# Kernel optimization log

Hardware: AMD Instinct MI355X
Metric: run time of the kernel (lower is better)

The kernel has to match this reference:

```python
import jax, jax.numpy as jnp
import numpy as np

D = 1024       # hidden_dim
H = 16         # n_heads
HD = D // H    # head dim = 64
V = 32000      # vocab_size
S = 4          # n_scales
IT = 6         # iters_per_scale
L = S * IT     # total_layers = 24 (one shared block, looped)
G = 16         # n_rot_groups
g = D // G     # group dim = 64
FF = 4 * D     # ff_mult * hidden_dim
N_TRI = g * (g - 1) // 2  # 2016 upper-tri skew params per group
EPS = 1e-6


def rmsnorm(x, w):
    return x * jax.lax.rsqrt(jnp.mean(x * x, axis=-1, keepdims=True) + EPS) * w


def setup_inputs() -> dict:
    key = jax.random.key(0)
    ks = jax.random.split(key, 12)
    rn = lambda k, shape, s: jax.random.normal(k, shape, jnp.float32) * s
    return {
        "tokens": jax.random.randint(ks[0], (1, 1024), 0, V),
        "embed_w": rn(ks[1], (V, D), 0.02),
        "lm_head_w": rn(ks[2], (V, D), 0.02),
        "norm_w": jnp.ones((D,), jnp.float32),
        "layer_gamma": 1.0 + rn(ks[3], (L, D), 0.02),
        "layer_beta": rn(ks[4], (L, D), 0.02),
        "iter_scale": 1.0 + rn(ks[5], (S, IT), 0.02),
        "skew_upper": rn(ks[6], (L, G, N_TRI), 0.02),
        "ln1_w": jnp.ones((D,), jnp.float32),
        "ln2_w": jnp.ones((D,), jnp.float32),
        "wqkv": rn(ks[7], (D, 3 * D), 0.02),
        "wo": rn(ks[8], (D, D), 0.02),
        "w1": rn(ks[9], (D, FF), 0.02),
        "w2": rn(ks[10], (FF, D), 0.02),
    }


def _rotations(skew_upper):
    """Cayley transform per layer/group: R = (I - A/2)^-1 (I + A/2), A skew-symm."""
    rows, cols = np.triu_indices(g, k=1)
    def one_layer(su):  # su: (G, N_TRI)
        A = jnp.zeros((G, g, g), su.dtype).at[:, rows, cols].set(su)
        A = A - jnp.swapaxes(A, -1, -2)
        I = jnp.eye(g, dtype=su.dtype)
        return jnp.linalg.solve(I - 0.5 * A, I + 0.5 * A)  # (G, g, g)
    return jax.vmap(one_layer)(skew_upper)  # (L, G, g, g)


def _block(x, gamma, beta, ln1_w, ln2_w, wqkv, wo, w1, w2):
    """Pre-norm causal transformer block with (gamma, beta) affine modulation."""
    B, T, _ = x.shape
    h = rmsnorm(x, ln1_w) * gamma + beta
    qkv = h @ wqkv  # (B, T, 3D)
    q, k, v = jnp.split(qkv, 3, axis=-1)
    q = q.reshape(B, T, H, HD)
    k = k.reshape(B, T, H, HD)
    v = v.reshape(B, T, H, HD)
    scores = jnp.einsum('bqhd,bkhd->bhqk', q, k) / np.sqrt(HD).astype(np.float32)
    causal = jnp.tril(jnp.ones((T, T), bool))
    scores = jnp.where(causal, scores, jnp.float32(-1e9))
    attn = jax.nn.softmax(scores, axis=-1)
    attn_out = jnp.einsum('bhqk,bkhd->bqhd', attn, v).reshape(B, T, D) @ wo
    x = x + attn_out
    x = x + jax.nn.gelu(rmsnorm(x, ln2_w) @ w1) @ w2
    return x


def reference(tokens, embed_w, lm_head_w, norm_w, layer_gamma, layer_beta,
              iter_scale, skew_upper, ln1_w, ln2_w, wqkv, wo, w1, w2):
    B, T = tokens.shape
    x = embed_w[tokens].astype(jnp.float32)  # (B, T, D)
    R = _rotations(skew_upper)               # (L, G, g, g)
    its = iter_scale.reshape(-1)             # (L,) scale index order matches loop
    for l in range(L):
        blk = _block(x, layer_gamma[l], layer_beta[l], ln1_w, ln2_w, wqkv, wo, w1, w2)
        x = x + (blk - x) * its[l]           # affine residual blend
        xg = x.reshape(B, T, G, g)
        x = jnp.einsum('btgi,gij->btgj', xg, R[l]).reshape(B, T, D)  # group rotation
    x = rmsnorm(x, norm_w)
    return x @ lm_head_w.T                   # (B, T, V) logits
```

## Files before the change

### kernel.cpp

```cpp
#include <hip/hip_runtime.h>
#include <hip/hip_bf16.h>
#include <math.h>

constexpr int kD = 1024;
constexpr int kH = 16;
constexpr int kV = 32000;
constexpr int kT = 1024;
constexpr int kG = 16;
constexpr int kFF = 4096;
constexpr int kL = 24;
constexpr int kNTRI = 2016;
#define EPSF 1e-6f
#define L2E 1.44269504088896f

typedef __bf16 bf16x8 __attribute__((ext_vector_type(8)));
typedef __bf16 bf16x4 __attribute__((ext_vector_type(4)));
typedef float f32x4 __attribute__((ext_vector_type(4)));

#define GLOAD16(g, l)                                                   \
  __builtin_amdgcn_global_load_lds(                                     \
      (const __attribute__((address_space(1))) void*)(g),               \
      (__attribute__((address_space(3))) void*)(l), 16, 0, 0)

__global__ __launch_bounds__(256) void cayley_kernel(const float* __restrict__ skew,
                                                     float* __restrict__ R) {
  int lg = blockIdx.x;
  int tid = threadIdx.x;
  int r = tid & 63, q = tid >> 6;
  __shared__ float Ms[64][65];
  __shared__ float Bs[64][65];
  const float* su = skew + (size_t)lg * kNTRI;
#pragma unroll
  for (int cc = 0; cc < 16; ++cc) {
    int c = q * 16 + cc;
    float a = 0.f;
    if (r < c) a = su[r * (127 - r) / 2 + (c - r - 1)];
    else if (r > c) a = -su[c * (127 - c) / 2 + (r - c - 1)];
    Ms[r][c] = (r == c ? 1.f : 0.f) - 0.5f * a;
    Bs[r][c] = (r == c ? 1.f : 0.f) + 0.5f * a;
  }
  __syncthreads();
  for (int k = 0; k < 64; ++k) {
    float ip = 1.f / Ms[k][k];
    float f = Ms[r][k];
    float beta = (r == k) ? (1.f - ip) : (f * ip);
    float mk[16], bk[16];
#pragma unroll
    for (int cc = 0; cc < 16; ++cc) {
      mk[cc] = Ms[k][q * 16 + cc];
      bk[cc] = Bs[k][q * 16 + cc];
    }
    __syncthreads();
#pragma unroll
    for (int cc = 0; cc < 16; ++cc) {
      int c = q * 16 + cc;
      Ms[r][c] -= beta * mk[cc];
      Bs[r][c] -= beta * bk[cc];
    }
    __syncthreads();
  }
  float* Ro = R + ((size_t)lg * 64 + r) * 64;
#pragma unroll
  for (int cc = 0; cc < 16; ++cc) Ro[q * 16 + cc] = Bs[r][q * 16 + cc];
}

__global__ __launch_bounds__(256) void embed_kernel(const int* __restrict__ tok,
                                                    const float* __restrict__ ew,
                                                    float* __restrict__ x) {
  int i = blockIdx.x * 256 + threadIdx.x;
  int t = i >> 8;
  int d4 = i & 255;
  int v = tok[t];
  reinterpret_cast<float4*>(x)[i] =
      reinterpret_cast<const float4*>(ew + (size_t)v * kD)[d4];
}

__global__ __launch_bounds__(256) void cast_kernel(const float* __restrict__ W,
                                                   __bf16* __restrict__ O) {
  size_t i = ((size_t)blockIdx.x * 256 + threadIdx.x) * 8;
  float4 f0 = *reinterpret_cast<const float4*>(W + i);
  float4 f1 = *reinterpret_cast<const float4*>(W + i + 4);
  bf16x8 v;
  v[0] = (__bf16)f0.x; v[1] = (__bf16)f0.y;
  v[2] = (__bf16)f0.z; v[3] = (__bf16)f0.w;
  v[4] = (__bf16)f1.x; v[5] = (__bf16)f1.y;
  v[6] = (__bf16)f1.z; v[7] = (__bf16)f1.w;
  *reinterpret_cast<bf16x8*>(O + i) = v;
}

__global__ __launch_bounds__(256) void convt_kernel(const float* __restrict__ W,
                                                    __bf16* __restrict__ WT,
                                                    int K, int N) {
  __shared__ float tile[64][65];
  int t = threadIdx.x;
  int n0 = blockIdx.x * 64, k0 = blockIdx.y * 64;
#pragma unroll
  for (int r = 0; r < 4; ++r) {
    int kr = r * 16 + (t >> 4);
    int nc = (t & 15) * 4;
    float4 v = *reinterpret_cast<const float4*>(&W[(size_t)(k0 + kr) * N + n0 + nc]);
    tile[kr][nc + 0] = v.x;
    tile[kr][nc + 1] = v.y;
    tile[kr][nc + 2] = v.z;
    tile[kr][nc + 3] = v.w;
  }
  __syncthreads();
#pragma unroll
  for (int r = 0; r < 2; ++r) {
    int idx = r * 256 + t;
    int nrow = idx >> 3, kc = (idx & 7) * 8;
    bf16x8 v;
#pragma unroll
    for (int j = 0; j < 8; ++j) v[j] = (__bf16)tile[kc + j][nrow];
    *reinterpret_cast<bf16x8*>(&WT[(size_t)(n0 + nrow) * K + k0 + kc]) = v;
  }
}

template <bool AFFINE>
__global__ __launch_bounds__(256) void rms_kernel(const float* __restrict__ x,
                                                  const float* __restrict__ w,
                                                  const float* __restrict__ gamma,
                                                  const float* __restrict__ beta,
                                                  __bf16* __restrict__ out) {
  int t = blockIdx.x, tid = threadIdx.x;
  __shared__ float red4[4];
  float4 xv = reinterpret_cast<const float4*>(x + (size_t)t * kD)[tid];
  float ss = xv.x * xv.x + xv.y * xv.y + xv.z * xv.z + xv.w * xv.w;
#pragma unroll
  for (int o = 1; o < 64; o <<= 1) ss += __shfl_xor(ss, o);
  if ((tid & 63) == 0) red4[tid >> 6] = ss;
  __syncthreads();
  float tot = red4[0] + red4[1] + red4[2] + red4[3];
  float rms = rsqrtf(tot / (float)kD + EPSF);
  float4 wv = reinterpret_cast<const float4*>(w)[tid];
  float o0 = xv.x * rms * wv.x;
  float o1 = xv.y * rms * wv.y;
  float o2 = xv.z * rms * wv.z;
  float o3 = xv.w * rms * wv.w;
  if (AFFINE) {
    float4 gv = reinterpret_cast<const float4*>(gamma)[tid];
    float4 bv = reinterpret_cast<const float4*>(beta)[tid];
    o0 = o0 * gv.x + bv.x;
    o1 = o1 * gv.y + bv.y;
    o2 = o2 * gv.z + bv.z;
    o3 = o3 * gv.w + bv.w;
  }
  bf16x4 ov;
  ov[0] = (__bf16)o0; ov[1] = (__bf16)o1; ov[2] = (__bf16)o2; ov[3] = (__bf16)o3;
  *reinterpret_cast<bf16x4*>(out + (size_t)t * kD + tid * 4) = ov;
}

__global__ __launch_bounds__(256) void rms_red_kernel(const float* __restrict__ x,
                                                      const float* __restrict__ p0,
                                                      const float* __restrict__ p1,
                                                      const float* __restrict__ w,
                                                      float* __restrict__ y,
                                                      __bf16* __restrict__ hb) {
  int t = blockIdx.x, tid = threadIdx.x;
  __shared__ float red4[4];
  size_t base = (size_t)t * kD;
  float4 xv = reinterpret_cast<const float4*>(x + base)[tid];
  float4 a = reinterpret_cast<const float4*>(p0 + base)[tid];
  float4 b = reinterpret_cast<const float4*>(p1 + base)[tid];
  float4 yv;
  yv.x = xv.x + a.x + b.x;
  yv.y = xv.y + a.y + b.y;
  yv.z = xv.z + a.z + b.z;
  yv.w = xv.w + a.w + b.w;
  reinterpret_cast<float4*>(y + base)[tid] = yv;
  float ss = yv.x * yv.x + yv.y * yv.y + yv.z * yv.z + yv.w * yv.w;
#pragma unroll
  for (int o = 1; o < 64; o <<= 1) ss += __shfl_xor(ss, o);
  if ((tid & 63) == 0) red4[tid >> 6] = ss;
  __syncthreads();
  float tot = red4[0] + red4[1] + red4[2] + red4[3];
  float rms = rsqrtf(tot / (float)kD + EPSF);
  float4 wv = reinterpret_cast<const float4*>(w)[tid];
  bf16x4 ov;
  ov[0] = (__bf16)(yv.x * rms * wv.x);
  ov[1] = (__bf16)(yv.y * rms * wv.y);
  ov[2] = (__bf16)(yv.z * rms * wv.z);
  ov[3] = (__bf16)(yv.w * rms * wv.w);
  *reinterpret_cast<bf16x4*>(hb + base + tid * 4) = ov;
}

template <int BM, int BN, int NW, int EPI, bool BF32, int KSPLIT = 1, bool DBUF = false>
__global__ __launch_bounds__(NW * 64) void gemm_kernel(
    const __bf16* __restrict__ A, const void* __restrict__ Bv,
    const float* res, void* __restrict__ Cv, int M, int N, int K) {
  constexpr int WCOLS = (NW == 4) ? 2 : 4;
  constexpr int FM = (BM / 2) / 16;
  constexpr int FN = (BN / WCOLS) / 16;
  constexpr int AISS = BM / 8 / NW;
  constexpr int BISS = BN / 8 / NW;
  constexpr int NI = AISS + BISS;
  __shared__ __bf16 As[(DBUF ? 2 : 1) * BM * 64];
  __shared__ __bf16 Bs[(DBUF ? 2 : 1) * BN * 64];
  char* AsB = (char*)As;
  char* BsB = (char*)Bs;
  int tid = threadIdx.x;
  int w = tid >> 6, lane = tid & 63;
  int mt = M / BM, nt = N / BN;
  int cpx = gridDim.x >> 3;
  int id = (blockIdx.x & 7) * cpx + (blockIdx.x >> 3);
  int ks_id = id / (mt * nt);
  int rem = id % (mt * nt);
  int bm = (rem % mt) * BM, bn = (rem / mt) * BN;
  int kbeg = ks_id * (K / KSPLIT), kend = kbeg + K / KSPLIT;
  int lrow = lane & 15, g = lane >> 4;
  int grow = lane >> 3;
  int gswz = ((lane & 7) ^ grow) * 8;
  int rsw = (lrow & 7) << 4;
  int wm = (NW == 4) ? (w >> 1) : (w >> 2);
  int wn = (NW == 4) ? (w & 1) : (w & 3);
  int wr = wm * (BM / 2), wc = wn * (BN / WCOLS);
  f32x4 acc[FM][FN] = {};
  const __bf16* B16 = (const __bf16*)Bv;
  const float* B32 = (const float*)Bv;

  auto stage = [&](int buf, int k0) {
#pragma unroll
    for (int i = 0; i < AISS; ++i) {
      int rbase = (i * NW + w) * 8;
      GLOAD16(&A[(size_t)(bm + rbase + grow) * K + k0 + gswz],
              &As[buf * BM * 64 + rbase * 64]);
    }
#pragma unroll
    for (int i = 0; i < BISS; ++i) {
      int rbase = (i * NW + w) * 8;
      GLOAD16(&B16[(size_t)(bn + rbase + grow) * K + k0 + gswz],
              &Bs[buf * BN * 64 + rbase * 64]);
    }
  };

  auto compute = [&](int buf) {
    int offA = buf * BM * 128, offB = buf * BN * 128;
#pragma unroll
    for (int ks = 0; ks < 2; ++ks) {
      bf16x8 af[FM], bg[FN];
#pragma unroll
      for (int i = 0; i < FM; ++i)
        af[i] = *reinterpret_cast<const bf16x8*>(
            AsB + offA + (wr + i * 16 + lrow) * 128 + ((ks * 64 + g * 16) ^ rsw));
#pragma unroll
      for (int j = 0; j < FN; ++j)
        bg[j] = *reinterpret_cast<const bf16x8*>(
            BsB + offB + (wc + j * 16 + lrow) * 128 + ((ks * 64 + g * 16) ^ rsw));
#pragma unroll
      for (int i = 0; i < FM; ++i)
#pragma unroll
        for (int j = 0; j < FN; ++j)
          acc[i][j] = __builtin_amdgcn_mfma_f32_16x16x32_bf16(af[i], bg[j],
                                                              acc[i][j], 0, 0, 0);
    }
  };

  if constexpr (DBUF && !BF32) {
    stage(0, kbeg);
    int cur = 0;
    for (int k0 = kbeg; k0 < kend; k0 += 64) {
      bool more = (k0 + 64 < kend);
      if (more) stage(cur ^ 1, k0 + 64);
      if (more) {
        if constexpr (NI == 2) asm volatile("s_waitcnt vmcnt(2)" ::: "memory");
        else if constexpr (NI == 3) asm volatile("s_waitcnt vmcnt(3)" ::: "memory");
        else if constexpr (NI == 4) asm volatile("s_waitcnt vmcnt(4)" ::: "memory");
        else if constexpr (NI == 6) asm volatile("s_waitcnt vmcnt(6)" ::: "memory");
        else asm volatile("s_waitcnt vmcnt(0)" ::: "memory");
      } else {
        asm volatile("s_waitcnt vmcnt(0)" ::: "memory");
      }
      __builtin_amdgcn_sched_barrier(0);
      __builtin_amdgcn_s_barrier();
      compute(cur);
      __builtin_amdgcn_s_barrier();
      cur ^= 1;
    }
  } else {
    for (int k0 = kbeg; k0 < kend; k0 += 64) {
      if (!BF32) {
        stage(0, k0);
      } else {
#pragma unroll
        for (int rrep = 0; rrep < BN * 8 / (NW * 64); ++rrep) {
          int cid = rrep * NW * 64 + tid;
          int row = cid >> 3, kc = (cid & 7) * 8;
          const float* src = &B32[(size_t)(bn + row) * K + k0 + kc];
          float4 f0 = *reinterpret_cast<const float4*>(src);
          float4 f1 = *reinterpret_cast<const float4*>(src + 4);
          bf16x8 v;
          v[0] = (__bf16)f0.x; v[1] = (__bf16)f0.y;
          v[2] = (__bf16)f0.z; v[3] = (__bf16)f0.w;
          v[4] = (__bf16)f1.x; v[5] = (__bf16)f1.y;
          v[6] = (__bf16)f1.z; v[7] = (__bf16)f1.w;
          int swc = ((cid & 7) ^ (row & 7)) * 16;
          *reinterpret_cast<bf16x8*>(BsB + row * 128 + swc) = v;
        }
#pragma unroll
        for (int i = 0; i < AISS; ++i) {
          int rbase = (i * NW + w) * 8;
          GLOAD16(&A[(size_t)(bm + rbase + grow) * K + k0 + gswz], &As[rbase * 64]);
        }
      }
      __syncthreads();
      compute(0);
      __syncthreads();
    }
  }

  float* Cp = (float*)Cv + (size_t)ks_id * M * N;
  int crow0 = bm + wr + g * 4;
  int ccol0 = bn + wc + lrow;
#pragma unroll
  for (int i = 0; i < FM; ++i) {
#pragma unroll
    for (int j = 0; j < FN; ++j) {
#pragma unroll
      for (int r = 0; r < 4; ++r) {
        int row = crow0 + i * 16 + r;
        int col = ccol0 + j * 16;
        size_t idx = (size_t)row * N + col;
        float v = acc[i][j][r];
        if (EPI == 1) v += res[idx];
        if (EPI == 2) {
          float u = v;
          float z = 0.7978845608028654f * (u + 0.044715f * u * u * u);
          float ez = exp2f(z * (2.f * L2E));
          v = u * ez / (1.f + ez);
        }
        if (EPI == 2 || EPI == 3) ((__bf16*)Cv)[idx] = (__bf16)v;
        else Cp[idx] = v;
      }
    }
  }
}

__global__ __launch_bounds__(256) void fattn_kernel(const __bf16* __restrict__ qkv,
                                                    __bf16* __restrict__ out) {
  __shared__ __bf16 Ks[2][64 * 64];
  __shared__ __bf16 Vt[2][64 * 64];
  __shared__ __bf16 Ps[4 * 16 * 64];
  int tid = threadIdx.x;
  int bq = blockIdx.x * 64;
  int h = blockIdx.y;
  int w = tid >> 6, lane = tid & 63;
  int g = lane >> 4, lr = lane & 15;

  bf16x8 qf[2];
  const __bf16* qbase = qkv + (size_t)(bq + w * 16 + lr) * (3 * kD) + h * 64;
#pragma unroll
  for (int ks = 0; ks < 2; ++ks) {
    bf16x8 v = *reinterpret_cast<const bf16x8*>(qbase + ks * 32 + g * 8);
#pragma unroll
    for (int j = 0; j < 8; ++j) qf[ks][j] = (__bf16)((float)v[j] * 0.125f);
  }

  f32x4 acc[4] = {};
  float m = -1e30f, lsum = 0.f;

  int srow = tid >> 2, sseg = tid & 3;
  int vk = tid & 63, vd0 = (tid >> 6) * 16;
  char* PwB = (char*)(Ps + w * (16 * 64));
  int psw = (lr & 7) << 4;

  bf16x8 ka, kb2, va, vb;
  int ntiles = bq / 64 + 1;

  {
    const __bf16* src = qkv + (size_t)(srow) * (3 * kD) + kD + h * 64 + sseg * 16;
    ka = *reinterpret_cast<const bf16x8*>(src);
    kb2 = *reinterpret_cast<const bf16x8*>(src + 8);
    const __bf16* vsrc = qkv + (size_t)(vk) * (3 * kD) + 2 * kD + h * 64 + vd0;
    va = *reinterpret_cast<const bf16x8*>(vsrc);
    vb = *reinterpret_cast<const bf16x8*>(vsrc + 8);
    char* KsB = (char*)Ks[0];
    char* VtB = (char*)Vt[0];
    int bc = sseg * 32, sw = (srow & 7) << 4;
    *reinterpret_cast<bf16x8*>(KsB + srow * 128 + (bc ^ sw)) = ka;
    *reinterpret_cast<bf16x8*>(KsB + srow * 128 + ((bc + 16) ^ sw)) = kb2;
#pragma unroll
    for (int i = 0; i < 8; ++i) {
      int d = vd0 + i;
      *((__bf16*)(VtB + d * 128 + ((vk * 2) ^ ((d & 7) << 4)))) = va[i];
      d = vd0 + 8 + i;
      *((__bf16*)(VtB + d * 128 + ((vk * 2) ^ ((d & 7) << 4)))) = vb[i];
    }
  }

  int cur = 0;
  for (int kt = 0; kt < ntiles; ++kt) {
    if (kt + 1 < ntiles) {
      const __bf16* src =
          qkv + (size_t)((kt + 1) * 64 + srow) * (3 * kD) + kD + h * 64 + sseg * 16;
      ka = *reinterpret_cast<const bf16x8*>(src);
      kb2 = *reinterpret_cast<const bf16x8*>(src + 8);
      const __bf16* vsrc =
          qkv + (size_t)((kt + 1) * 64 + vk) * (3 * kD) + 2 * kD + h * 64 + vd0;
      va = *reinterpret_cast<const bf16x8*>(vsrc);
      vb = *reinterpret_cast<const bf16x8*>(vsrc + 8);
    }
    __syncthreads();

    char* KsB = (char*)Ks[cur];
    char* VtB = (char*)Vt[cur];
    bool diag = (kt == ntiles - 1);
    int jmax = diag ? w : 3;

    f32x4 s[4];
#pragma unroll
    for (int jj = 0; jj < 4; ++jj) {
      if (jj <= jmax) {
        int krow = jj * 16 + lr;
        int ksw = (lr & 7) << 4;
        bf16x8 k0 = *reinterpret_cast<const bf16x8*>(KsB + krow * 128 + ((g * 16) ^ ksw));
        bf16x8 k1 = *reinterpret_cast<const bf16x8*>(KsB + krow * 128 + ((64 + g * 16) ^ ksw));
        f32x4 z = {};
        z = __builtin_amdgcn_mfma_f32_16x16x32_bf16(k0, qf[0], z, 0, 0, 0);
        s[jj] = __builtin_amdgcn_mfma_f32_16x16x32_bf16(k1, qf[1], z, 0, 0, 0);
      } else {
        s[jj] = f32x4{-1e30f, -1e30f, -1e30f, -1e30f};
      }
    }
    if (diag) {
#pragma unroll
      for (int r = 0; r < 4; ++r)
        if (g * 4 + r > lr) s[w][r] = -1e30f;
    }

    float mt = -1e30f;
#pragma unroll
    for (int jj = 0; jj < 4; ++jj)
#pragma unroll
      for (int r = 0; r < 4; ++r) mt = fmaxf(mt, s[jj][r]);
    mt = fmaxf(mt, __shfl_xor(mt, 16));
    mt = fmaxf(mt, __shfl_xor(mt, 32));
    float mn = fmaxf(m, mt);
    float sc = exp2f((m - mn) * L2E);
    float p[4][4];
    float rs = 0.f;
#pragma unroll
    for (int jj = 0; jj < 4; ++jj)
#pragma unroll
      for (int r = 0; r < 4; ++r) {
        float e = exp2f((s[jj][r] - mn) * L2E);
        p[jj][r] = e;
        rs += e;
      }
    rs += __shfl_xor(rs, 16);
    rs += __shfl_xor(rs, 32);
    lsum = lsum * sc + rs;
    m = mn;
#pragma unroll
    for (int r = 0; r < 4; ++r) {
      float s4 = __shfl(sc, 20 * g + r);
#pragma unroll
      for (int dt = 0; dt < 4; ++dt) acc[dt][r] *= s4;
    }

#pragma unroll
    for (int jj = 0; jj < 4; ++jj) {
      bf16x4 pv;
#pragma unroll
      for (int r = 0; r < 4; ++r) pv[r] = (__bf16)p[jj][r];
      *reinterpret_cast<bf16x4*>(PwB + lr * 128 + ((jj * 32 + g * 8) ^ psw)) = pv;
    }

    {
      bf16x8 pa0 = *reinterpret_cast<const bf16x8*>(PwB + lr * 128 + ((g * 16) ^ psw));
      bf16x8 pa1 = *reinterpret_cast<const bf16x8*>(PwB + lr * 128 + ((64 + g * 16) ^ psw));
#pragma unroll
      for (int dt = 0; dt < 4; ++dt) {
        int vrow = dt * 16 + lr;
        int vsw = (lr & 7) << 4;
        bf16x8 vb0 = *reinterpret_cast<const bf16x8*>(VtB + vrow * 128 + ((g * 16) ^ vsw));
        bf16x8 vb1 = *reinterpret_cast<const bf16x8*>(VtB + vrow * 128 + ((64 + g * 16) ^ vsw));
        acc[dt] = __builtin_amdgcn_mfma_f32_16x16x32_bf16(pa0, vb0, acc[dt], 0, 0, 0);
        acc[dt] = __builtin_amdgcn_mfma_f32_16x16x32_bf16(pa1, vb1, acc[dt], 0, 0, 0);
      }
    }
    __syncthreads();

    if (kt + 1 < ntiles) {
      char* KsN = (char*)Ks[cur ^ 1];
      char* VtN = (char*)Vt[cur ^ 1];
      int bc = sseg * 32, sw = (srow & 7) << 4;
      *reinterpret_cast<bf16x8*>(KsN + srow * 128 + (bc ^ sw)) = ka;
      *reinterpret_cast<bf16x8*>(KsN + srow * 128 + ((bc + 16) ^ sw)) = kb2;
#pragma unroll
      for (int i = 0; i < 8; ++i) {
        int d = vd0 + i;
        *((__bf16*)(VtN + d * 128 + ((vk * 2) ^ ((d & 7) << 4)))) = va[i];
        d = vd0 + 8 + i;
        *((__bf16*)(VtN + d * 128 + ((vk * 2) ^ ((d & 7) << 4)))) = vb[i];
      }
      cur ^= 1;
    }
  }

  float linv = 1.f / lsum;
#pragma unroll
  for (int r = 0; r < 4; ++r) {
    float ir = __shfl(linv, 20 * g + r);
    int row = bq + w * 16 + g * 4 + r;
#pragma unroll
    for (int dt = 0; dt < 4; ++dt)
      out[(size_t)row * kD + h * 64 + dt * 16 + lr] = (__bf16)(acc[dt][r] * ir);
  }
}

__global__ __launch_bounds__(256) void blend_rot_kernel(const float* x,
                                                        const float* y,
                                                        const float* q0,
                                                        const float* q1,
                                                        const float* iscale,
                                                        int l,
                                                        const float* __restrict__ Rall,
                                                        float* xout) {
  int tc = blockIdx.x, gr = blockIdx.y;
  int tid = threadIdx.x;
  __shared__ float Rs[64 * 64];
  __shared__ float xb[64][65];
  float s = iscale[l];
  const float* Rg = Rall + ((size_t)l * kG + gr) * 4096;
  {
    int off = tid * 16;
#pragma unroll
    for (int q2 = 0; q2 < 4; ++q2) {
      float4 rv = *reinterpret_cast<const float4*>(Rg + off + q2 * 4);
      *reinterpret_cast<float4*>(&Rs[off + q2 * 4]) = rv;
    }
  }
  int tok = tid & 63, seg = (tid >> 6) * 16;
  {
    size_t base = (size_t)(tc * 64 + tok) * kD + gr * 64 + seg;
#pragma unroll
    for (int q2 = 0; q2 < 4; ++q2) {
      float4 xv = *reinterpret_cast<const float4*>(x + base + q2 * 4);
      float4 yv = *reinterpret_cast<const float4*>(y + base + q2 * 4);
      float4 a = *reinterpret_cast<const float4*>(q0 + base + q2 * 4);
      float4 b = *reinterpret_cast<const float4*>(q1 + base + q2 * 4);
      float y0 = yv.x + a.x + b.x;
      float y1 = yv.y + a.y + b.y;
      float y2 = yv.z + a.z + b.z;
      float y3 = yv.w + a.w + b.w;
      xb[tok][seg + q2 * 4 + 0] = xv.x + (y0 - xv.x) * s;
      xb[tok][seg + q2 * 4 + 1] = xv.y + (y1 - xv.y) * s;
      xb[tok][seg + q2 * 4 + 2] = xv.z + (y2 - xv.z) * s;
      xb[tok][seg + q2 * 4 + 3] = xv.w + (y3 - xv.w) * s;
    }
  }
  __syncthreads();
  float o[16] = {};
  for (int i = 0; i < 64; ++i) {
    float xv = xb[tok][i];
#pragma unroll
    for (int d = 0; d < 16; ++d) o[d] += xv * Rs[i * 64 + seg + d];
  }
  float* outr = xout + (size_t)(tc * 64 + tok) * kD + gr * 64 + seg;
#pragma unroll
  for (int q2 = 0; q2 < 4; ++q2) {
    float4 ov = {o[q2 * 4 + 0], o[q2 * 4 + 1], o[q2 * 4 + 2], o[q2 * 4 + 3]};
    *reinterpret_cast<float4*>(outr + q2 * 4) = ov;
  }
}

extern "C" void kernel_launch(void* const* d_in, const int* in_sizes, int n_in,
                              void* d_out, int out_size, void* d_ws, size_t ws_size,
                              hipStream_t stream) {
  const int* tokens = (const int*)d_in[0];
  const float* embed_w = (const float*)d_in[1];
  const float* lm_head_w = (const float*)d_in[2];
  const float* norm_w = (const float*)d_in[3];
  const float* layer_gamma = (const float*)d_in[4];
  const float* layer_beta = (const float*)d_in[5];
  const float* iter_scale = (const float*)d_in[6];
  const float* skew_upper = (const float*)d_in[7];
  const float* ln1_w = (const float*)d_in[8];
  const float* ln2_w = (const float*)d_in[9];
  const float* wqkv = (const float*)d_in[10];
  const float* wo = (const float*)d_in[11];
  const float* w1 = (const float*)d_in[12];
  const float* w2 = (const float*)d_in[13];
  float* out = (float*)d_out;

  float* x = (float*)d_ws;
  float* y = x + (size_t)kT * kD;
  __bf16* hb = (__bf16*)(y + (size_t)kT * kD);
  __bf16* ab = hb + (size_t)kT * kD;
  float* R = (float*)(ab + (size_t)kT * kD);
  __bf16* lmhb = (__bf16*)(R + (size_t)kL * kG * 4096);
  bool ws_big = ws_size >= (size_t)(4670464 + 16384000) * 4;

  __bf16* qkvb = (__bf16*)out;
  __bf16* ffb = (__bf16*)(out + 1572864);
  __bf16* wqkvT = (__bf16*)(out + 3670016);
  __bf16* woT = (__bf16*)(out + 5242880);
  __bf16* w1T = (__bf16*)(out + 5767168);
  __bf16* w2T = (__bf16*)(out + 7864320);
  float* wop = out + 9961472;
  float* w2p = out + 12058624;

  cayley_kernel<<<kL * kG, 256, 0, stream>>>(skew_upper, R);
  embed_kernel<<<kT * kD / 4 / 256, 256, 0, stream>>>(tokens, embed_w, x);
  convt_kernel<<<dim3(3 * kD / 64, kD / 64), 256, 0, stream>>>(wqkv, wqkvT, kD, 3 * kD);
  convt_kernel<<<dim3(kD / 64, kD / 64), 256, 0, stream>>>(wo, woT, kD, kD);
  convt_kernel<<<dim3(kFF / 64, kD / 64), 256, 0, stream>>>(w1, w1T, kD, kFF);
  convt_kernel<<<dim3(kD / 64, kFF / 64), 256, 0, stream>>>(w2, w2T, kFF, kD);
  if (ws_big)
    cast_kernel<<<kV * kD / 8 / 256, 256, 0, stream>>>(lm_head_w, lmhb);

  for (int l = 0; l < kL; ++l) {
    rms_kernel<true><<<kT, 256, 0, stream>>>(x, ln1_w, layer_gamma + (size_t)l * kD,
                                             layer_beta + (size_t)l * kD, hb);
    gemm_kernel<64, 128, 8, 3, false, 1, true>
        <<<(kT / 64) * (3 * kD / 128), 512, 0, stream>>>(
        hb, wqkvT, nullptr, qkvb, kT, 3 * kD, kD);
    fattn_kernel<<<dim3(kT / 64, kH), 256, 0, stream>>>(qkvb, ab);
    gemm_kernel<64, 64, 8, 0, false, 2, true>
        <<<2 * (kT / 64) * (kD / 64), 512, 0, stream>>>(
        ab, woT, nullptr, wop, kT, kD, kD);
    rms_red_kernel<<<kT, 256, 0, stream>>>(x, wop, wop + (size_t)kT * kD, ln2_w, y, hb);
    gemm_kernel<64, 128, 8, 2, false, 1, true>
        <<<(kT / 64) * (kFF / 128), 512, 0, stream>>>(
        hb, w1T, nullptr, ffb, kT, kFF, kD);
    gemm_kernel<64, 64, 8, 0, false, 2, true>
        <<<2 * (kT / 64) * (kD / 64), 512, 0, stream>>>(
        ffb, w2T, nullptr, w2p, kT, kD, kFF);
    blend_rot_kernel<<<dim3(kT / 64, kG), 256, 0, stream>>>(
        x, y, w2p, w2p + (size_t)kT * kD, iter_scale, l, R, x);
  }

  rms_kernel<false><<<kT, 256, 0, stream>>>(x, norm_w, nullptr, nullptr, hb);
  if (ws_big)
    gemm_kernel<256, 128, 8, 0, false><<<(kT / 256) * (kV / 128), 512, 0, stream>>>(
        hb, lmhb, nullptr, out, kT, kV, kD);
  else
    gemm_kernel<128, 128, 4, 0, true><<<(kT / 128) * (kV / 128), 256, 0, stream>>>(
        hb, lm_head_w, nullptr, out, kT, kV, kD);
}
```

Before: 2.578 ms.

## Split causal attention KV range in two halves with a combine kernel

The flash attention kernel now splits each query tile's causal key range into two halves across separate blocks, writing unnormalized fp32 partial accumulators plus row max and sum to scratch. A new combine kernel merges the two halves with log-sum-exp rescaling and writes the bf16 output. Block indices are remapped so that heads are grouped per XCD, and the grid doubles to 512 blocks to balance the triangular workload. The cost is an extra kernel launch and fp32 partial traffic through global memory on every layer.

```diff
diff --git a/kernel.cpp b/kernel.cpp
--- a/kernel.cpp
+++ b/kernel.cpp
@@ -336,15 +336,36 @@
 }
 
 __global__ __launch_bounds__(256) void fattn_kernel(const __bf16* __restrict__ qkv,
-                                                    __bf16* __restrict__ out) {
+                                                    float* __restrict__ pacc,
+                                                    float* __restrict__ pm,
+                                                    float* __restrict__ pl) {
   __shared__ __bf16 Ks[2][64 * 64];
   __shared__ __bf16 Vt[2][64 * 64];
   __shared__ __bf16 Ps[4 * 16 * 64];
+  int b = blockIdx.x;
+  int xcd = b & 7, idx = b >> 3;
+  int h = xcd * 2 + (idx >> 5);
+  int rem2 = idx & 31;
+  int qt = rem2 >> 1, half = rem2 & 1;
+  int bq = qt * 64;
+  int ntk = qt + 1;
+  int kb = half ? (ntk >> 1) : 0;
+  int ke = half ? ntk : (ntk >> 1);
+  int tix = (qt * 16 + h) * 2 + half;
   int tid = threadIdx.x;
-  int bq = blockIdx.x * 64;
-  int h = blockIdx.y;
   int w = tid >> 6, lane = tid & 63;
   int g = lane >> 4, lr = lane & 15;
+
+  if (kb >= ke) {
+    float* pa = pacc + (size_t)tix * 4096;
+#pragma unroll
+    for (int i = 0; i < 16; ++i) pa[tid * 16 + i] = 0.f;
+    if (tid < 64) {
+      pm[tix * 64 + tid] = -1e30f;
+      pl[tix * 64 + tid] = 0.f;
+    }
+    return;
+  }
 
   bf16x8 qf[2];
   const __bf16* qbase = qkv + (size_t)(bq + w * 16 + lr) * (3 * kD) + h * 64;
@@ -364,13 +385,12 @@
   int psw = (lr & 7) << 4;
 
   bf16x8 ka, kb2, va, vb;
-  int ntiles = bq / 64 + 1;
 
   {
-    const __bf16* src = qkv + (size_t)(srow) * (3 * kD) + kD + h * 64 + sseg * 16;
+    const __bf16* src = qkv + (size_t)(kb * 64 + srow) * (3 * kD) + kD + h * 64 + sseg * 16;
     ka = *reinterpret_cast<const bf16x8*>(src);
     kb2 = *reinterpret_cast<const bf16x8*>(src + 8);
-    const __bf16* vsrc = qkv + (size_t)(vk) * (3 * kD) + 2 * kD + h * 64 + vd0;
+    const __bf16* vsrc = qkv + (size_t)(kb * 64 + vk) * (3 * kD) + 2 * kD + h * 64 + vd0;
     va = *reinterpret_cast<const bf16x8*>(vsrc);
     vb = *reinterpret_cast<const bf16x8*>(vsrc + 8);
     char* KsB = (char*)Ks[0];
@@ -388,8 +408,8 @@
   }
 
   int cur = 0;
-  for (int kt = 0; kt < ntiles; ++kt) {
-    if (kt + 1 < ntiles) {
+  for (int kt = kb; kt < ke; ++kt) {
+    if (kt + 1 < ke) {
       const __bf16* src =
           qkv + (size_t)((kt + 1) * 64 + srow) * (3 * kD) + kD + h * 64 + sseg * 16;
       ka = *reinterpret_cast<const bf16x8*>(src);
@@ -403,7 +423,7 @@
 
     char* KsB = (char*)Ks[cur];
     char* VtB = (char*)Vt[cur];
-    bool diag = (kt == ntiles - 1);
+    bool diag = (kt == qt);
     int jmax = diag ? w : 3;
 
     f32x4 s[4];
@@ -480,7 +500,7 @@
     }
     __syncthreads();
 
-    if (kt + 1 < ntiles) {
+    if (kt + 1 < ke) {
       char* KsN = (char*)Ks[cur ^ 1];
       char* VtN = (char*)Vt[cur ^ 1];
       int bc = sseg * 32, sw = (srow & 7) << 4;
@@ -497,14 +517,45 @@
     }
   }
 
-  float linv = 1.f / lsum;
+  float* pa = pacc + (size_t)tix * 4096;
 #pragma unroll
   for (int r = 0; r < 4; ++r) {
-    float ir = __shfl(linv, 20 * g + r);
-    int row = bq + w * 16 + g * 4 + r;
+    int row = w * 16 + g * 4 + r;
 #pragma unroll
     for (int dt = 0; dt < 4; ++dt)
-      out[(size_t)row * kD + h * 64 + dt * 16 + lr] = (__bf16)(acc[dt][r] * ir);
+      pa[row * 64 + dt * 16 + lr] = acc[dt][r];
+  }
+  if (g == 0) {
+    pm[tix * 64 + w * 16 + lr] = m;
+    pl[tix * 64 + w * 16 + lr] = lsum;
+  }
+}
+
+__global__ __launch_bounds__(256) void fattn_combine_kernel(
+    const float* __restrict__ pacc, const float* __restrict__ pm,
+    const float* __restrict__ pl, __bf16* __restrict__ ab) {
+  int qt = blockIdx.x, h = blockIdx.y;
+  int tid = threadIdx.x;
+  int row = tid >> 2, c0 = (tid & 3) * 16;
+  int t0 = (qt * 16 + h) * 2, t1 = t0 + 1;
+  float m0 = pm[t0 * 64 + row], m1 = pm[t1 * 64 + row];
+  float l0 = pl[t0 * 64 + row], l1 = pl[t1 * 64 + row];
+  float mm = fmaxf(m0, m1);
+  float e0 = exp2f((m0 - mm) * L2E), e1 = exp2f((m1 - mm) * L2E);
+  float inv = 1.f / (e0 * l0 + e1 * l1);
+  const float* a0 = pacc + (size_t)t0 * 4096 + row * 64 + c0;
+  const float* a1 = pacc + (size_t)t1 * 4096 + row * 64 + c0;
+  __bf16* o = ab + (size_t)(qt * 64 + row) * kD + h * 64 + c0;
+#pragma unroll
+  for (int c = 0; c < 16; c += 4) {
+    float4 v0 = *reinterpret_cast<const float4*>(a0 + c);
+    float4 v1 = *reinterpret_cast<const float4*>(a1 + c);
+    bf16x4 ov;
+    ov[0] = (__bf16)((e0 * v0.x + e1 * v1.x) * inv);
+    ov[1] = (__bf16)((e0 * v0.y + e1 * v1.y) * inv);
+    ov[2] = (__bf16)((e0 * v0.z + e1 * v1.z) * inv);
+    ov[3] = (__bf16)((e0 * v0.w + e1 * v1.w) * inv);
+    *reinterpret_cast<bf16x4*>(o + c) = ov;
   }
 }
 
@@ -599,6 +650,9 @@
   __bf16* w2T = (__bf16*)(out + 7864320);
   float* wop = out + 9961472;
   float* w2p = out + 12058624;
+  float* pacc = out + 14155776;
+  float* pm = out + 16252928;
+  float* pl = out + 16285696;
 
   cayley_kernel<<<kL * kG, 256, 0, stream>>>(skew_upper, R);
   embed_kernel<<<kT * kD / 4 / 256, 256, 0, stream>>>(tokens, embed_w, x);
@@ -615,7 +669,8 @@
     gemm_kernel<64, 128, 8, 3, false, 1, true>
         <<<(kT / 64) * (3 * kD / 128), 512, 0, stream>>>(
         hb, wqkvT, nullptr, qkvb, kT, 3 * kD, kD);
-    fattn_kernel<<<dim3(kT / 64, kH), 256, 0, stream>>>(qkvb, ab);
+    fattn_kernel<<<512, 256, 0, stream>>>(qkvb, pacc, pm, pl);
+    fattn_combine_kernel<<<dim3(kT / 64, kH), 256, 0, stream>>>(pacc, pm, pl, ab);
     gemm_kernel<64, 64, 8, 0, false, 2, true>
         <<<2 * (kT / 64) * (kD / 64), 512, 0, stream>>>(
         ab, woT, nullptr, wop, kT, kD, kD);
```

After: 2.567 ms, median of 2. No clear change (-0.4%).
